# Kernel tuning notes

Hardware: AMD Instinct MI355X
Metric: run time of the kernel (lower is better)

## Reference

```python
import jax, jax.numpy as jnp
import numpy as np

DK = 128
B, S = 16, 2048

def setup_inputs() -> dict:
    key = jax.random.key(0)
    kq, kk, kv = jax.random.split(key, 3)
    q = jax.random.normal(kq, (B, S, DK), dtype=jnp.float32)
    k = jax.random.normal(kk, (B, S, DK), dtype=jnp.float32)
    v = jax.random.normal(kv, (B, S, DK), dtype=jnp.float32)
    return {"q": q, "k": k, "v": v}

def reference(q, k, v):
    # scores: [B, S, S]
    scale = 1.0 / jnp.sqrt(jnp.float32(DK))
    scores = jnp.einsum("bqd,bkd->bqk", q, k) * scale
    probs = jax.nn.softmax(scores, axis=-1)
    # dropout is identity in eval mode (training=None)
    return jnp.einsum("bqk,bkd->bqd", probs, v)
```

## Files before the change

kernel.cpp:

```cpp
#include <hip/hip_runtime.h>
#include <hip/hip_bf16.h>

#define BATCH 16
#define SEQ   2048
#define DK    128
#define NT    16
#define SC2   0.12751744f
#define THRL2 11.541560f

typedef __attribute__((ext_vector_type(8)))  short short8v;
typedef __attribute__((ext_vector_type(4)))  float float4v;
typedef __attribute__((ext_vector_type(16))) float float16v;

typedef const __attribute__((address_space(1))) unsigned int* gas_t;
typedef __attribute__((address_space(3))) unsigned int* las_t;

__device__ inline void gl_lds16(const void* g, void* l) {
    __builtin_amdgcn_global_load_lds((gas_t)g, (las_t)l, 16, 0, 0);
}

__device__ inline short f2bf(float f) {
    __hip_bfloat16 h = __float2bfloat16(f);
    unsigned short u;
    __builtin_memcpy(&u, &h, sizeof(u));
    return (short)u;
}

__device__ inline unsigned cvt_pk_bf16(float a, float b) {
    unsigned r;
    asm("v_cvt_pk_bf16_f32 %0, %1, %2" : "=v"(r) : "v"(a), "v"(b));
    return r;
}

__global__ __launch_bounds__(256)
void conv_k_kernel(const float* __restrict__ k, short* __restrict__ kb)
{
    size_t i = ((size_t)blockIdx.x * 256 + threadIdx.x) * 8;
    float4 a = *reinterpret_cast<const float4*>(k + i);
    float4 b = *reinterpret_cast<const float4*>(k + i + 4);
    short8v t;
    t[0] = f2bf(a.x * SC2); t[1] = f2bf(a.y * SC2); t[2] = f2bf(a.z * SC2); t[3] = f2bf(a.w * SC2);
    t[4] = f2bf(b.x * SC2); t[5] = f2bf(b.y * SC2); t[6] = f2bf(b.z * SC2); t[7] = f2bf(b.w * SC2);
    *reinterpret_cast<short8v*>(kb + i) = t;
}

__global__ __launch_bounds__(256)
void transpose_v_kernel(const float* __restrict__ v, short* __restrict__ vt)
{
    __shared__ float tile[32][33];
    const int tx = threadIdx.x & 31;
    const int ty = threadIdx.x >> 5;
    const int b  = blockIdx.z;
    const int s0 = blockIdx.x * 32;
    const int d0 = blockIdx.y * 32;

    const float* vb = v + ((size_t)b * SEQ + s0) * DK + d0;
#pragma unroll
    for (int i = 0; i < 4; ++i) {
        int r = ty + 8 * i;
        tile[r][tx] = vb[(size_t)r * DK + tx];
    }
    __syncthreads();

    const int s   = s0 + tx;
    const int kvl = s & 15;
    const int pos = (((kvl >> 2) & 1) << 3) | (((kvl >> 3) & 1) << 2) | (kvl & 3);
    const size_t col = (size_t)(s & ~15) | pos;

    short* vtb = vt + ((size_t)b * DK + d0) * SEQ;
#pragma unroll
    for (int i = 0; i < 4; ++i) {
        int r = ty + 8 * i;
        vtb[(size_t)r * SEQ + col] = f2bf(tile[tx][r]);
    }
}

__global__ __launch_bounds__(512, 2)
void attn_fwd_v13(const float* __restrict__ q,
                  const short* __restrict__ kb,
                  const short* __restrict__ vt,
                  float* __restrict__ out)
{
    __shared__ __align__(16) char lds[131072];

    const int tid  = threadIdx.x;
    const int lane = tid & 63;
    const int wave = tid >> 6;
    const int qt   = wave & 3;
    const int h    = wave >> 2;
    const int bid  = blockIdx.x;
    const int work = (bid & 7) * 32 + (bid >> 3);
    const int b    = work >> 4;
    const int q0   = (work & 15) * 128 + qt * 32;

    const int l31 = lane & 31;
    const int hi  = lane >> 5;

    const float* qrow = q + ((size_t)b * SEQ + q0 + l31) * DK + hi * 8;
    short8v qf[8];
#pragma unroll
    for (int s = 0; s < 8; ++s) {
        float4 x = *reinterpret_cast<const float4*>(qrow + s * 16);
        float4 y = *reinterpret_cast<const float4*>(qrow + s * 16 + 4);
        union { unsigned u[4]; short8v v; } pk;
        pk.u[0] = cvt_pk_bf16(x.x, x.y);
        pk.u[1] = cvt_pk_bf16(x.z, x.w);
        pk.u[2] = cvt_pk_bf16(y.x, y.y);
        pk.u[3] = cvt_pk_bf16(y.z, y.w);
        qf[s] = pk.v;
    }

    const char* kB = (const char*)(kb + (size_t)b * SEQ * DK);
    const char* vB = (const char*)(vt + (size_t)b * DK * SEQ);
    const int hkv = h * 1024;

    const char* src[8];
    int dstoff[8];
    long sstep;
    if (qt < 2) {
#pragma unroll
        for (int i = 0; i < 8; ++i) {
            const int kr = qt * 32 + i * 4 + (lane >> 4);
            src[i] = kB + (size_t)(hkv + kr) * 256 + (((lane & 15) ^ (kr & 15)) << 4);
            dstoff[i] = h * 32768 + qt * 8192 + i * 1024;
        }
        sstep = 64 * 256;
    } else {
#pragma unroll
        for (int i = 0; i < 8; ++i) {
            const int R  = (qt - 2) * 32 + i * 4 + (lane >> 4);
            const int wx = (lane & 15) ^ (R & 15);
            const int d  = 2 * R + (wx >> 3);
            src[i] = vB + (size_t)d * (SEQ * 2) + (size_t)hkv * 2 + ((wx & 7) << 4);
            dstoff[i] = h * 32768 + 16384 + (qt - 2) * 8192 + i * 1024;
        }
        sstep = 64 * 2;
    }

    float m_run = -1e30f;
    float l_run = 0.0f;
    float16v o[4];
#pragma unroll
    for (int dblk = 0; dblk < 4; ++dblk)
#pragma unroll
        for (int i = 0; i < 16; ++i) o[dblk][i] = 0.f;

    auto STAGE = [&](int bufsel, int t) {
        char* base = lds + bufsel * 65536;
#pragma unroll
        for (int i = 0; i < 8; ++i)
            gl_lds16(src[i] + (size_t)t * sstep, base + dstoff[i]);
    };

    STAGE(0, 0);
    __syncthreads();

    int buf = 0;
    for (int t = 0; t < NT; ++t) {
        if (t + 1 < NT) STAGE(buf ^ 1, t + 1);

        const char* Kl = lds + buf * 65536 + h * 32768;
        const char* Vl = Kl + 16384;
        const char* ka = Kl + l31 * 256;

        float16v sa[2];
#pragma unroll
        for (int i = 0; i < 16; ++i) { sa[0][i] = 0.f; sa[1][i] = 0.f; }
        __builtin_amdgcn_s_setprio(1);
#pragma unroll
        for (int s = 0; s < 8; ++s) {
            const int un = ((2 * s + hi) ^ (l31 & 15)) << 4;
            short8v kf0 = *reinterpret_cast<const short8v*>(ka + un);
            short8v kf1 = *reinterpret_cast<const short8v*>(ka + 8192 + un);
            sa[0] = __builtin_amdgcn_mfma_f32_32x32x16_bf16(kf0, qf[s], sa[0], 0, 0, 0);
            sa[1] = __builtin_amdgcn_mfma_f32_32x32x16_bf16(kf1, qf[s], sa[1], 0, 0, 0);
        }
        __builtin_amdgcn_s_setprio(0);

        float mx = sa[0][0];
#pragma unroll
        for (int i = 1; i < 16; ++i) mx = fmaxf(mx, sa[0][i]);
#pragma unroll
        for (int i = 0; i < 16; ++i) mx = fmaxf(mx, sa[1][i]);
        mx = fmaxf(mx, __shfl_xor(mx, 32));

        if (!__all(mx <= m_run + THRL2)) {
            const float mnew  = fmaxf(m_run, mx);
            const float alpha = exp2f(m_run - mnew);
            l_run *= alpha;
            m_run = mnew;
            float aq[16];
#pragma unroll
            for (int reg = 0; reg < 16; ++reg)
                aq[reg] = __shfl(alpha, (reg & 3) + 8 * (reg >> 2) + 4 * hi);
#pragma unroll
            for (int dblk = 0; dblk < 4; ++dblk)
#pragma unroll
                for (int reg = 0; reg < 16; ++reg) o[dblk][reg] *= aq[reg];
        }

        float ts = 0.f;
#pragma unroll
        for (int sub = 0; sub < 2; ++sub)
#pragma unroll
            for (int i = 0; i < 16; ++i) {
                const float e = exp2f(sa[sub][i] - m_run);
                sa[sub][i] = e;
                ts += e;
            }
        ts += __shfl_xor(ts, 32);
        l_run += ts;

        short8v pf[4];
#pragma unroll
        for (int g = 0; g < 4; ++g) {
            const int sub = g >> 1, r0 = (g & 1) * 8;
            union { unsigned u[4]; short8v v; } pk;
            pk.u[0] = cvt_pk_bf16(sa[sub][r0 + 0], sa[sub][r0 + 1]);
            pk.u[1] = cvt_pk_bf16(sa[sub][r0 + 2], sa[sub][r0 + 3]);
            pk.u[2] = cvt_pk_bf16(sa[sub][r0 + 4], sa[sub][r0 + 5]);
            pk.u[3] = cvt_pk_bf16(sa[sub][r0 + 6], sa[sub][r0 + 7]);
            pf[g] = pk.v;
        }

        __builtin_amdgcn_s_setprio(1);
#pragma unroll
        for (int dblk = 0; dblk < 4; ++dblk) {
            const int R  = dblk * 16 + (l31 >> 1);
            const char* vr = Vl + R * 256;
            const int dh = (l31 & 1) << 3;
#pragma unroll
            for (int g = 0; g < 4; ++g) {
                const int w = ((dh | (2 * g + hi)) ^ (R & 15)) << 4;
                short8v vf = *reinterpret_cast<const short8v*>(vr + w);
                o[dblk] = __builtin_amdgcn_mfma_f32_32x32x16_bf16(pf[g], vf, o[dblk], 0, 0, 0);
            }
        }
        __builtin_amdgcn_s_setprio(0);

        __syncthreads();
        buf ^= 1;
    }

    float* smO = (float*)lds;
    float* smM = (float*)(lds + 65536);
    float* smL = (float*)(lds + 66048);

    if (h == 1) {
        if (hi == 0) { smM[qt * 32 + l31] = m_run; smL[qt * 32 + l31] = l_run; }
#pragma unroll
        for (int dblk = 0; dblk < 4; ++dblk)
#pragma unroll
            for (int reg = 0; reg < 16; ++reg) {
                const int qp = (reg & 3) + 8 * (reg >> 2) + 4 * hi;
                smO[(qt * 32 + qp) * 128 + dblk * 32 + l31] = o[dblk][reg];
            }
    }
    __syncthreads();
    if (h == 0) {
        const float m1 = smM[qt * 32 + l31];
        const float l1 = smL[qt * 32 + l31];
        const float mf = fmaxf(m_run, m1);
        const float a0 = exp2f(m_run - mf);
        const float a1 = exp2f(m1 - mf);
        const float li = 1.0f / (l_run * a0 + l1 * a1);
        const float w0 = a0 * li;
        const float w1 = a1 * li;

        float w0q[16], w1q[16];
#pragma unroll
        for (int reg = 0; reg < 16; ++reg) {
            const int qp = (reg & 3) + 8 * (reg >> 2) + 4 * hi;
            w0q[reg] = __shfl(w0, qp);
            w1q[reg] = __shfl(w1, qp);
        }

        float* ob = out + ((size_t)b * SEQ + q0) * DK;
#pragma unroll
        for (int dblk = 0; dblk < 4; ++dblk)
#pragma unroll
            for (int reg = 0; reg < 16; ++reg) {
                const int qp = (reg & 3) + 8 * (reg >> 2) + 4 * hi;
                ob[(size_t)qp * DK + dblk * 32 + l31] =
                    o[dblk][reg] * w0q[reg]
                    + smO[(qt * 32 + qp) * 128 + dblk * 32 + l31] * w1q[reg];
            }
    }
}

__global__ __launch_bounds__(256)
void attn_fwd_slow(const float* __restrict__ q,
                   const float* __restrict__ k,
                   const float* __restrict__ v,
                   float* __restrict__ out)
{
    const int lane = threadIdx.x & 63;
    const int wave = threadIdx.x >> 6;
    const int b    = blockIdx.y;
    const int q0   = blockIdx.x * 64 + wave * 16;
    const int row = lane & 15;
    const int grp = lane >> 4;

    const float* qb = q + ((size_t)b * SEQ + q0) * DK;
    const float* kbp = k + (size_t)b * SEQ * DK;
    const float* vbp = v + (size_t)b * SEQ * DK;

    short8v qf[4];
#pragma unroll
    for (int c = 0; c < 4; ++c) {
        const float* p = qb + row * DK + c * 32 + grp * 8;
        float4 x = *reinterpret_cast<const float4*>(p);
        float4 y = *reinterpret_cast<const float4*>(p + 4);
        short8v t;
        t[0] = f2bf(x.x); t[1] = f2bf(x.y); t[2] = f2bf(x.z); t[3] = f2bf(x.w);
        t[4] = f2bf(y.x); t[5] = f2bf(y.y); t[6] = f2bf(y.z); t[7] = f2bf(y.w);
        qf[c] = t;
    }

    float m_run = -1e30f, l_run = 0.0f;
    float4v o[8];
#pragma unroll
    for (int i = 0; i < 8; ++i) { o[i][0]=0.f; o[i][1]=0.f; o[i][2]=0.f; o[i][3]=0.f; }
    const float scale = 0.08838834764831845f;

    for (int kv0 = 0; kv0 < SEQ; kv0 += 16) {
        short8v kf[4];
        const float* kp0 = kbp + (size_t)(kv0 + row) * DK + grp * 8;
#pragma unroll
        for (int c = 0; c < 4; ++c) {
            const float* p = kp0 + c * 32;
            float4 x = *reinterpret_cast<const float4*>(p);
            float4 y = *reinterpret_cast<const float4*>(p + 4);
            short8v t;
            t[0] = f2bf(x.x); t[1] = f2bf(x.y); t[2] = f2bf(x.z); t[3] = f2bf(x.w);
            t[4] = f2bf(y.x); t[5] = f2bf(y.y); t[6] = f2bf(y.z); t[7] = f2bf(y.w);
            kf[c] = t;
        }
        short8v vf[8];
#pragma unroll
        for (int dblk = 0; dblk < 8; ++dblk) {
            const float* p = vbp + (size_t)(kv0 + 4 * grp) * DK + dblk * 16 + row;
            short b0 = f2bf(p[0]);
            short b1 = f2bf(p[DK]);
            short b2 = f2bf(p[2 * DK]);
            short b3 = f2bf(p[3 * DK]);
            short8v t;
            t[0]=b0; t[1]=b1; t[2]=b2; t[3]=b3; t[4]=b0; t[5]=b1; t[6]=b2; t[7]=b3;
            vf[dblk] = t;
        }
        float4v s; s[0]=0.f; s[1]=0.f; s[2]=0.f; s[3]=0.f;
#pragma unroll
        for (int c = 0; c < 4; ++c)
            s = __builtin_amdgcn_mfma_f32_16x16x32_bf16(kf[c], qf[c], s, 0, 0, 0);

        float sv[4]; float tmax = -1e30f;
#pragma unroll
        for (int r = 0; r < 4; ++r) { sv[r] = s[r] * scale; tmax = fmaxf(tmax, sv[r]); }
        tmax = fmaxf(tmax, __shfl_xor(tmax, 16));
        tmax = fmaxf(tmax, __shfl_xor(tmax, 32));
        const float mnew = fmaxf(m_run, tmax);
        float pr[4]; float tsum = 0.f;
#pragma unroll
        for (int r = 0; r < 4; ++r) { pr[r] = __expf(sv[r] - mnew); tsum += pr[r]; }
        tsum += __shfl_xor(tsum, 16);
        tsum += __shfl_xor(tsum, 32);
        const float alpha = __expf(m_run - mnew);
        l_run = l_run * alpha + tsum;
        m_run = mnew;
        float aq[4];
#pragma unroll
        for (int r = 0; r < 4; ++r) aq[r] = __shfl(alpha, grp * 4 + r);
#pragma unroll
        for (int dblk = 0; dblk < 8; ++dblk)
#pragma unroll
            for (int r = 0; r < 4; ++r) o[dblk][r] *= aq[r];

        short8v pfv;
        pfv[0]=f2bf(pr[0]); pfv[1]=f2bf(pr[1]); pfv[2]=f2bf(pr[2]); pfv[3]=f2bf(pr[3]);
        pfv[4]=0; pfv[5]=0; pfv[6]=0; pfv[7]=0;
#pragma unroll
        for (int dblk = 0; dblk < 8; ++dblk)
            o[dblk] = __builtin_amdgcn_mfma_f32_16x16x32_bf16(pfv, vf[dblk], o[dblk], 0, 0, 0);
    }

    const float linv = 1.0f / l_run;
    float li[4];
#pragma unroll
    for (int r = 0; r < 4; ++r) li[r] = __shfl(linv, grp * 4 + r);
    float* ob = out + ((size_t)b * SEQ + q0) * DK;
#pragma unroll
    for (int dblk = 0; dblk < 8; ++dblk)
#pragma unroll
        for (int r = 0; r < 4; ++r)
            ob[(size_t)(grp * 4 + r) * DK + dblk * 16 + row] = o[dblk][r] * li[r];
}

extern "C" void kernel_launch(void* const* d_in, const int* in_sizes, int n_in,
                              void* d_out, int out_size, void* d_ws, size_t ws_size,
                              hipStream_t stream) {
    const float* q = (const float*)d_in[0];
    const float* k = (const float*)d_in[1];
    const float* v = (const float*)d_in[2];
    float* out = (float*)d_out;

    const size_t kb_bytes = (size_t)BATCH * SEQ * DK * sizeof(short);
    const size_t need = 2 * kb_bytes;

    if (ws_size >= need) {
        short* kb = (short*)d_ws;
        short* vt = (short*)((char*)d_ws + kb_bytes);
        hipLaunchKernelGGL(conv_k_kernel, dim3(2048), dim3(256), 0, stream, k, kb);
        hipLaunchKernelGGL(transpose_v_kernel, dim3(SEQ / 32, DK / 32, BATCH), dim3(256), 0, stream, v, vt);
        hipLaunchKernelGGL(attn_fwd_v13, dim3((SEQ / 128) * BATCH), dim3(512), 0, stream, q, kb, vt, out);
    } else {
        hipLaunchKernelGGL(attn_fwd_slow, dim3(SEQ / 64, BATCH), dim3(256), 0, stream, q, k, v, out);
    }
}
```

Before: 67.78 us.

## Fuse K convert and V transpose prepasses, vectorize V stores, tree-reduce softmax

Merges the K bf16 conversion and the V transpose into one prepass launch, removing one kernel launch and its tail. The V transpose now writes packed 8-byte bf16 groups per thread instead of scattered 2-byte stores. In the attention kernel, the row max becomes a tree reduction and the exp sum uses four partial accumulators, shortening the dependency chains. These add some index arithmetic, and the fused launch mixes two kinds of block work in one grid.

```diff
diff --git a/kernel.cpp b/kernel.cpp
--- a/kernel.cpp
+++ b/kernel.cpp
@@ -33,50 +33,57 @@
 }
 
 __global__ __launch_bounds__(256)
-void conv_k_kernel(const float* __restrict__ k, short* __restrict__ kb)
+void prepass_kernel(const float* __restrict__ k, const float* __restrict__ v,
+                    short* __restrict__ kb, short* __restrict__ vt)
 {
-    size_t i = ((size_t)blockIdx.x * 256 + threadIdx.x) * 8;
-    float4 a = *reinterpret_cast<const float4*>(k + i);
-    float4 b = *reinterpret_cast<const float4*>(k + i + 4);
-    short8v t;
-    t[0] = f2bf(a.x * SC2); t[1] = f2bf(a.y * SC2); t[2] = f2bf(a.z * SC2); t[3] = f2bf(a.w * SC2);
-    t[4] = f2bf(b.x * SC2); t[5] = f2bf(b.y * SC2); t[6] = f2bf(b.z * SC2); t[7] = f2bf(b.w * SC2);
-    *reinterpret_cast<short8v*>(kb + i) = t;
-}
-
-__global__ __launch_bounds__(256)
-void transpose_v_kernel(const float* __restrict__ v, short* __restrict__ vt)
-{
+    if (blockIdx.x < 2048) {
+        size_t i = ((size_t)blockIdx.x * 256 + threadIdx.x) * 8;
+        float4 a = *reinterpret_cast<const float4*>(k + i);
+        float4 b = *reinterpret_cast<const float4*>(k + i + 4);
+        short8v t;
+        t[0] = f2bf(a.x * SC2); t[1] = f2bf(a.y * SC2); t[2] = f2bf(a.z * SC2); t[3] = f2bf(a.w * SC2);
+        t[4] = f2bf(b.x * SC2); t[5] = f2bf(b.y * SC2); t[6] = f2bf(b.z * SC2); t[7] = f2bf(b.w * SC2);
+        *reinterpret_cast<short8v*>(kb + i) = t;
+        return;
+    }
+
     __shared__ float tile[32][33];
+    const int vb_ = blockIdx.x - 2048;
+    const int b   = vb_ >> 8;
+    const int st  = (vb_ >> 2) & 63;
+    const int dt  = vb_ & 3;
+    const int s0  = st * 32;
+    const int d0  = dt * 32;
+
     const int tx = threadIdx.x & 31;
     const int ty = threadIdx.x >> 5;
-    const int b  = blockIdx.z;
-    const int s0 = blockIdx.x * 32;
-    const int d0 = blockIdx.y * 32;
-
-    const float* vb = v + ((size_t)b * SEQ + s0) * DK + d0;
+    const float* vbp = v + ((size_t)b * SEQ + s0) * DK + d0;
 #pragma unroll
     for (int i = 0; i < 4; ++i) {
         int r = ty + 8 * i;
-        tile[r][tx] = vb[(size_t)r * DK + tx];
+        tile[r][tx] = vbp[(size_t)r * DK + tx];
     }
     __syncthreads();
 
-    const int s   = s0 + tx;
-    const int kvl = s & 15;
-    const int pos = (((kvl >> 2) & 1) << 3) | (((kvl >> 3) & 1) << 2) | (kvl & 3);
-    const size_t col = (size_t)(s & ~15) | pos;
-
-    short* vtb = vt + ((size_t)b * DK + d0) * SEQ;
-#pragma unroll
-    for (int i = 0; i < 4; ++i) {
-        int r = ty + 8 * i;
-        vtb[(size_t)r * SEQ + col] = f2bf(tile[tx][r]);
-    }
+    const int d  = threadIdx.x >> 3;
+    const int g2 = (threadIdx.x >> 2) & 1;
+    const int qq = threadIdx.x & 3;
+    const int kvb = g2 * 16 + ((qq >> 1) << 2) + ((qq & 1) << 3);
+
+    const float f0 = tile[kvb + 0][d];
+    const float f1 = tile[kvb + 1][d];
+    const float f2 = tile[kvb + 2][d];
+    const float f3 = tile[kvb + 3][d];
+    union { unsigned u[2]; unsigned long long ll; } pk;
+    pk.u[0] = cvt_pk_bf16(f0, f1);
+    pk.u[1] = cvt_pk_bf16(f2, f3);
+
+    short* o = vt + ((size_t)b * DK + d0 + d) * SEQ + s0 + g2 * 16 + qq * 4;
+    *reinterpret_cast<unsigned long long*>(o) = pk.ll;
 }
 
 __global__ __launch_bounds__(512, 2)
-void attn_fwd_v13(const float* __restrict__ q,
+void attn_fwd_v14(const float* __restrict__ q,
                   const short* __restrict__ kb,
                   const short* __restrict__ vt,
                   float* __restrict__ out)
@@ -177,12 +184,14 @@
         }
         __builtin_amdgcn_s_setprio(0);
 
-        float mx = sa[0][0];
-#pragma unroll
-        for (int i = 1; i < 16; ++i) mx = fmaxf(mx, sa[0][i]);
-#pragma unroll
-        for (int i = 0; i < 16; ++i) mx = fmaxf(mx, sa[1][i]);
-        mx = fmaxf(mx, __shfl_xor(mx, 32));
+        float t16[16];
+#pragma unroll
+        for (int i = 0; i < 16; ++i) t16[i] = fmaxf(sa[0][i], sa[1][i]);
+#pragma unroll
+        for (int s2 = 8; s2 > 0; s2 >>= 1)
+#pragma unroll
+            for (int i = 0; i < s2; ++i) t16[i] = fmaxf(t16[i], t16[i + s2]);
+        float mx = fmaxf(t16[0], __shfl_xor(t16[0], 32));
 
         if (!__all(mx <= m_run + THRL2)) {
             const float mnew  = fmaxf(m_run, mx);
@@ -199,15 +208,16 @@
                 for (int reg = 0; reg < 16; ++reg) o[dblk][reg] *= aq[reg];
         }
 
-        float ts = 0.f;
+        float ts4[4] = {0.f, 0.f, 0.f, 0.f};
 #pragma unroll
         for (int sub = 0; sub < 2; ++sub)
 #pragma unroll
             for (int i = 0; i < 16; ++i) {
                 const float e = exp2f(sa[sub][i] - m_run);
                 sa[sub][i] = e;
-                ts += e;
+                ts4[i & 3] += e;
             }
+        float ts = (ts4[0] + ts4[1]) + (ts4[2] + ts4[3]);
         ts += __shfl_xor(ts, 32);
         l_run += ts;
 
@@ -407,11 +417,10 @@
     const size_t need = 2 * kb_bytes;
 
     if (ws_size >= need) {
-        short* kb = (short*)d_ws;
-        short* vt = (short*)((char*)d_ws + kb_bytes);
-        hipLaunchKernelGGL(conv_k_kernel, dim3(2048), dim3(256), 0, stream, k, kb);
-        hipLaunchKernelGGL(transpose_v_kernel, dim3(SEQ / 32, DK / 32, BATCH), dim3(256), 0, stream, v, vt);
-        hipLaunchKernelGGL(attn_fwd_v13, dim3((SEQ / 128) * BATCH), dim3(512), 0, stream, q, kb, vt, out);
+        short* kbuf = (short*)d_ws;
+        short* vtbuf = (short*)((char*)d_ws + kb_bytes);
+        hipLaunchKernelGGL(prepass_kernel, dim3(2048 + 4096), dim3(256), 0, stream, k, v, kbuf, vtbuf);
+        hipLaunchKernelGGL(attn_fwd_v14, dim3((SEQ / 128) * BATCH), dim3(512), 0, stream, q, kbuf, vtbuf, out);
     } else {
         hipLaunchKernelGGL(attn_fwd_slow, dim3(SEQ / 64, BATCH), dim3(256), 0, stream, q, k, v, out);
     }
```

Result: faster. 63.19 us (-6.8%).
